# Optimization experiments

Measured on AMD Instinct MI355X. Metric: run time of the kernel, lower is better.

The kernel has to match this reference:

```python
import jax, jax.numpy as jnp
import numpy as np

B, L, C, D = 8, 8192, 256, 256


def setup_inputs() -> dict:
    key = jax.random.key(0)
    ks = jax.random.split(key, 13)
    bound = 1.0 / np.sqrt(C)

    def W(k):
        return jax.random.uniform(k, (C, D), jnp.float32, -bound, bound)

    def b(k):
        return jax.random.uniform(k, (D,), jnp.float32, -bound, bound)

    return {
        "xs": jax.random.normal(ks[0], (B, L, C), jnp.float32),
        # forward-direction params
        "Wh1": W(ks[1]), "bh1": b(ks[2]),
        "Wz1": W(ks[3]), "bz1": b(ks[4]),
        "Ws1": W(ks[5]), "bs1": b(ks[6]),
        "h01": jnp.zeros((1, 1, D), jnp.float32),
        # backward-direction params
        "Wh_1": W(ks[7]), "bh_1": b(ks[8]),
        "Wz_1": W(ks[9]), "bz_1": b(ks[10]),
        "Ws_1": W(ks[11]), "bs_1": b(ks[12]),
        "h0_1": jnp.zeros((1, 1, D), jnp.float32),
    }


def _gru_scan(z, h_tilde, h0):
    """h[t] = z[t]*h_tilde[t] + (1-z[t])*h[t-1], h[-1]=h0. Parallel over time
    via associative scan on the affine maps h -> a*h + b."""
    a = 1.0 - z            # [B, L, D]
    b = z * h_tilde        # [B, L, D]

    def combine(c1, c2):
        a1, b1 = c1
        a2, b2 = c2
        return a1 * a2, a2 * b1 + b2

    A, Bc = jax.lax.associative_scan(combine, (a, b), axis=1)
    return Bc + A * h0     # broadcast h0 [1,1,D]


def reference(xs, Wh1, bh1, Wz1, bz1, Ws1, bs1, h01,
              Wh_1, bh_1, Wz_1, bz_1, Ws_1, bs_1, h0_1):
    sig = jax.nn.sigmoid
    # forward direction
    hf = _gru_scan(sig(xs @ Wz1 + bz1), xs @ Wh1 + bh1, h01) * sig(xs @ Ws1 + bs1)
    # backward direction: reverse time, scan, reverse back
    zr = sig(xs @ Wz_1 + bz_1)
    hr = xs @ Wh_1 + bh_1
    hb = _gru_scan(zr[:, ::-1], hr[:, ::-1], h0_1)[:, ::-1] * sig(xs @ Ws_1 + bs_1)
    return hf + hb
```

## Files before the change

kernel.cpp:

```cpp
#include <hip/hip_runtime.h>
#include <hip/hip_bf16.h>

typedef unsigned short u16;

#define BDIM 8
#define LDIM 8192
#define KDIM 256
#define DDIM 256
#define MTOT 65536
#define NDIM 1536
#define TCH  32
#define NCH  256
#define NSUP 16


typedef float floatx4 __attribute__((ext_vector_type(4)));
typedef short bf16x8 __attribute__((ext_vector_type(8)));
typedef unsigned int u32x4 __attribute__((ext_vector_type(4)));
typedef unsigned int u32x2 __attribute__((ext_vector_type(2)));

__device__ __forceinline__ u16 f2bf(float f) {
  union { __hip_bfloat16 h; u16 u; } c;
  c.h = __float2bfloat16(f);
  return c.u;
}
__device__ __forceinline__ float bf2f(u16 u) {
  union { unsigned int i; float f; } c;
  c.i = ((unsigned int)u) << 16;
  return c.f;
}
__device__ __forceinline__ float sigmoidf_fast(float x) {
  return __builtin_amdgcn_rcpf(1.0f + __expf(-x));
}
__device__ __forceinline__ void gll16(const u16* g, u16* l) {
  __builtin_amdgcn_global_load_lds((const __attribute__((address_space(1))) void*)g,
                                   (__attribute__((address_space(3))) void*)l, 16, 0, 0);
}

__global__ void prep_conv(const float* __restrict__ Wh1, const float* __restrict__ Wz1,
                          const float* __restrict__ Ws1, const float* __restrict__ Wh_1,
                          const float* __restrict__ Wz_1, const float* __restrict__ Ws_1,
                          const float* __restrict__ bh1, const float* __restrict__ bz1,
                          const float* __restrict__ bs1, const float* __restrict__ bh_1,
                          const float* __restrict__ bz_1, const float* __restrict__ bs_1,
                          u16* __restrict__ WcatT, float* __restrict__ bcat,
                          const float* __restrict__ xs, u16* __restrict__ Abf) {
  if (blockIdx.x < NDIM) {
    const int n = blockIdx.x;
    const int k = threadIdx.x;
    const int nn = n & 63;
    const int p = (n & ~63) | ((nn & 15) << 2) | (nn >> 4);
    const int dir = p / 768, r = p % 768;
    int d; const float* W; const float* bb;
    if (r < 512) {
      d = r >> 1;
      if (r & 1) { W = dir ? Wz_1 : Wz1; bb = dir ? bz_1 : bz1; }
      else       { W = dir ? Wh_1 : Wh1; bb = dir ? bh_1 : bh1; }
    } else {
      d = r - 512;
      W = dir ? Ws_1 : Ws1; bb = dir ? bs_1 : bs1;
    }
    WcatT[(size_t)n * KDIM + k] = f2bf(W[k * DDIM + d]);
    if (k == 0) bcat[p] = bb[d];
  } else {
    const int cb = blockIdx.x - NDIM;
#pragma unroll
    for (int pass = 0; pass < 4; ++pass) {
      size_t i = ((size_t)(pass * 2048 + cb) * 256 + threadIdx.x) * 8;
      const float4* s = (const float4*)(xs + i);
      float4 f0 = s[0], f1 = s[1];
      union { u16 u[8]; u32x4 v; } t;
      t.u[0] = f2bf(f0.x); t.u[1] = f2bf(f0.y); t.u[2] = f2bf(f0.z); t.u[3] = f2bf(f0.w);
      t.u[4] = f2bf(f1.x); t.u[5] = f2bf(f1.y); t.u[6] = f2bf(f1.z); t.u[7] = f2bf(f1.w);
      *(u32x4*)(Abf + i) = t.v;
    }
  }
}

__global__ __launch_bounds__(256) void gemm_kernel(const u16* __restrict__ Abf,
                                                   const u16* __restrict__ WcatT,
                                                   const float* __restrict__ bcat,
                                                   u16* __restrict__ G,
                                                   float* __restrict__ Acc,
                                                   float* __restrict__ Bcc) {
  __shared__ __align__(16) u16 sm[16384];
  u16* As = sm;
  u16* Bs = sm + 8192;
  const int tid = threadIdx.x;
  const int lane = tid & 63, wave = tid >> 6;
  const int wm = wave >> 1, wn = wave & 1;
  const int q = lane >> 4, r = lane & 15;

  const int xcd = blockIdx.x & 7;
  const int li  = blockIdx.x >> 3;
  const int mt  = xcd * 64 + li / 12;
  const int nt  = li % 12;
  const int m0 = mt * 128, n0 = nt * 128;

  const u16* gA[4]; const u16* gB[4]; u16* lA[4]; u16* lB[4];
#pragma unroll
  for (int j = 0; j < 4; j++) {
    const int bi = wave * 256 + j * 64 + lane;
    const int row = bi >> 3;
    const int kq = (bi & 7) ^ (row & 7);
    gA[j] = Abf   + (size_t)(m0 + row) * KDIM + kq * 8;
    gB[j] = WcatT + (size_t)(n0 + row) * KDIM + kq * 8;
    lA[j] = As + bi * 8;
    lB[j] = Bs + bi * 8;
  }

  floatx4 acc[4][4];
  floatx4 z4 = {0.f, 0.f, 0.f, 0.f};
#pragma unroll
  for (int i = 0; i < 4; i++)
#pragma unroll
    for (int j = 0; j < 4; j++) acc[i][j] = z4;

  for (int k0 = 0; k0 < KDIM; k0 += 64) {
#pragma unroll
    for (int j = 0; j < 4; j++) { gll16(gA[j] + k0, lA[j]); gll16(gB[j] + k0, lB[j]); }
    __syncthreads();
#pragma unroll
    for (int kk = 0; kk < 2; kk++) {
      bf16x8 af[4], bv[4];
#pragma unroll
      for (int i = 0; i < 4; i++) {
        const int row = wm * 64 + i * 16 + r;
        af[i] = *(const bf16x8*)(As + (row * 8 + ((kk * 4 + q) ^ (row & 7))) * 8);
      }
#pragma unroll
      for (int j = 0; j < 4; j++) {
        const int row = wn * 64 + j * 16 + r;
        bv[j] = *(const bf16x8*)(Bs + (row * 8 + ((kk * 4 + q) ^ (row & 7))) * 8);
      }
#pragma unroll
      for (int i = 0; i < 4; i++)
#pragma unroll
        for (int j = 0; j < 4; j++)
          acc[i][j] = __builtin_amdgcn_mfma_f32_16x16x32_bf16(af[i], bv[j], acc[i][j], 0, 0, 0);
    }
    __syncthreads();
  }

  const int pcol = wn * 64 + (r << 2);
  const float4 bv4 = *(const float4*)(bcat + n0 + pcol);
  const int hz = (n0 % 768) < 512;

  if (hz) {
#pragma unroll
    for (int i = 0; i < 4; i++) {
#pragma unroll
      for (int reg = 0; reg < 4; reg++) {
        const int lrow = wm * 64 + i * 16 + q * 4 + reg;
        union { u16 u[4]; u32x2 v; } t;
        t.u[0] = f2bf(acc[i][0][reg] + bv4.x);
        t.u[1] = f2bf(acc[i][1][reg] + bv4.y);
        t.u[2] = f2bf(acc[i][2][reg] + bv4.z);
        t.u[3] = f2bf(acc[i][3][reg] + bv4.w);
        *(u32x2*)(sm + lrow * 128 + pcol) = t.v;
      }
    }

    __syncthreads();

#pragma unroll
    for (int p = 0; p < 8; p++) {
      const int idx = p * 2048 + tid * 8;
      const int row = idx >> 7, col = idx & 127;
      const u32x4 v = *(const u32x4*)(sm + idx);
      *(u32x4*)(G + (size_t)(m0 + row) * NDIM + n0 + col) = v;
    }

    const int cc = wave;
    const int dd = lane;
    const int dirn = n0 / 768;
    const int dbase = (n0 % 768) >> 1;
    const int bb = m0 >> 13;
    const int c0 = (m0 & 8191) >> 5;
    float h = 0.f, P = 1.f;
#pragma unroll 8
    for (int i = 0; i < TCH; ++i) {
      const int tl = dirn ? (TCH - 1 - i) : i;
      const unsigned int hzv = *(const unsigned int*)(sm + (cc * 32 + tl) * 128 + dd * 2);
      const float z = sigmoidf_fast(bf2f((u16)(hzv >> 16)));
      const float a = 1.f - z;
      h = fmaf(a, h, z * bf2f((u16)(hzv & 0xffffu)));
      P *= a;
    }
    const size_t u = (size_t)dirn * 2048 + (size_t)bb * 256 + (size_t)(c0 + cc);
    Acc[u * 256 + dbase + dd] = P;
    Bcc[u * 256 + dbase + dd] = h;
  } else {
#pragma unroll
    for (int i = 0; i < 4; i++) {
#pragma unroll
      for (int reg = 0; reg < 4; reg++) {
        const int lrow = wm * 64 + i * 16 + q * 4 + reg;
        union { u16 u[4]; u32x2 v; } t;
        t.u[0] = f2bf(acc[i][0][reg] + bv4.x);
        t.u[1] = f2bf(acc[i][1][reg] + bv4.y);
        t.u[2] = f2bf(acc[i][2][reg] + bv4.z);
        t.u[3] = f2bf(acc[i][3][reg] + bv4.w);
        *(u32x2*)(G + (size_t)(m0 + lrow) * NDIM + n0 + pcol) = t.v;
      }
    }
  }
}

__global__ __launch_bounds__(256) void scan_phaseB1(float* __restrict__ Acc,
                                                    float* __restrict__ Bcc,
                                                    float* __restrict__ Asum,
                                                    float* __restrict__ Bsum) {
  const int d = threadIdx.x;
  const int s   = blockIdx.x & 15;
  const int b   = (blockIdx.x >> 4) & 7;
  const int dir = blockIdx.x >> 7;
  const size_t ubase = ((size_t)dir * BDIM + b) * NCH;
  float a[16], bb[16];
#pragma unroll
  for (int i = 0; i < 16; ++i) {
    const int c = dir ? (NCH - 1 - (s * 16 + i)) : (s * 16 + i);
    const size_t idx = (ubase + c) * DDIM + d;
    a[i] = Acc[idx]; bb[i] = Bcc[idx];
  }
  float A = 1.f, Bv = 0.f;
#pragma unroll
  for (int i = 0; i < 16; ++i) {
    const int c = dir ? (NCH - 1 - (s * 16 + i)) : (s * 16 + i);
    const size_t idx = (ubase + c) * DDIM + d;
    Acc[idx] = A; Bcc[idx] = Bv;
    Bv = fmaf(a[i], Bv, bb[i]);
    A  = a[i] * A;
  }
  const size_t sidx = (((size_t)dir * BDIM + b) * NSUP + s) * DDIM + d;
  Asum[sidx] = A; Bsum[sidx] = Bv;
}

__global__ __launch_bounds__(256) void scan_phaseC(const u16* __restrict__ G,
                                                   const float* __restrict__ Acc,
                                                   const float* __restrict__ Bcc,
                                                   const float* __restrict__ Asum,
                                                   const float* __restrict__ Bsum,
                                                   const float* __restrict__ h01,
                                                   const float* __restrict__ h0_1,
                                                   float* __restrict__ out) {
  __shared__ float obuf[TCH * 256];
  const int c = blockIdx.x & 255, b = blockIdx.x >> 8;
  const int dir = threadIdx.x >> 7;
  const int ld  = threadIdx.x & 127;
  const int d0 = ld * 2;

  const int sp = dir ? ((NCH - 1 - c) >> 4) : (c >> 4);
  const float2 hh = dir ? *(const float2*)(h0_1 + d0) : *(const float2*)(h01 + d0);
  float ha = hh.x, hb = hh.y;
  const size_t sbase = ((size_t)dir * BDIM + b) * NSUP;
  for (int s = 0; s < sp; ++s) {
    const float2 As2 = *(const float2*)(Asum + (sbase + s) * DDIM + d0);
    const float2 Bs2 = *(const float2*)(Bsum + (sbase + s) * DDIM + d0);
    ha = fmaf(As2.x, ha, Bs2.x);
    hb = fmaf(As2.y, hb, Bs2.y);
  }
  const int u = dir * 2048 + b * 256 + c;
  const float2 ap = *(const float2*)(Acc + (size_t)u * 256 + d0);
  const float2 bp = *(const float2*)(Bcc + (size_t)u * 256 + d0);
  float h0 = fmaf(ap.x, ha, bp.x);
  float h1 = fmaf(ap.y, hb, bp.y);

  const u16* ghz = G + (size_t)b * LDIM * NDIM + dir * 768 + d0 * 2;
  const u16* gs  = G + (size_t)b * LDIM * NDIM + dir * 768 + 512 + d0;

  {
    uint2 hzr[16]; unsigned int sr[16];
#pragma unroll
    for (int i = 0; i < 16; ++i) {
      const int tl = dir ? (TCH - 1 - i) : i;
      const int t = c * TCH + tl;
      hzr[i] = *(const uint2*)(ghz + (size_t)t * NDIM);
      sr[i]  = *(const unsigned int*)(gs + (size_t)t * NDIM);
    }
#pragma unroll
    for (int i = 0; i < 16; ++i) {
      const int tl = dir ? (TCH - 1 - i) : i;
      const float z0 = sigmoidf_fast(bf2f((u16)(hzr[i].x >> 16)));
      const float z1 = sigmoidf_fast(bf2f((u16)(hzr[i].y >> 16)));
      h0 = fmaf(1.f - z0, h0, z0 * bf2f((u16)(hzr[i].x & 0xffffu)));
      h1 = fmaf(1.f - z1, h1, z1 * bf2f((u16)(hzr[i].y & 0xffffu)));
      float2 o;
      o.x = h0 * sigmoidf_fast(bf2f((u16)(sr[i] & 0xffffu)));
      o.y = h1 * sigmoidf_fast(bf2f((u16)(sr[i] >> 16)));
      *(float2*)(obuf + tl * 256 + d0) = o;
    }
  }

  __syncthreads();

  {
    uint2 hzr[16]; unsigned int sr[16];
#pragma unroll
    for (int i = 0; i < 16; ++i) {
      const int tl = dir ? (TCH - 1 - (16 + i)) : (16 + i);
      const int t = c * TCH + tl;
      hzr[i] = *(const uint2*)(ghz + (size_t)t * NDIM);
      sr[i]  = *(const unsigned int*)(gs + (size_t)t * NDIM);
    }
#pragma unroll
    for (int i = 0; i < 16; ++i) {
      const int tl = dir ? (TCH - 1 - (16 + i)) : (16 + i);
      const int t = c * TCH + tl;
      const float z0 = sigmoidf_fast(bf2f((u16)(hzr[i].x >> 16)));
      const float z1 = sigmoidf_fast(bf2f((u16)(hzr[i].y >> 16)));
      h0 = fmaf(1.f - z0, h0, z0 * bf2f((u16)(hzr[i].x & 0xffffu)));
      h1 = fmaf(1.f - z1, h1, z1 * bf2f((u16)(hzr[i].y & 0xffffu)));
      const float o0 = h0 * sigmoidf_fast(bf2f((u16)(sr[i] & 0xffffu)));
      const float o1 = h1 * sigmoidf_fast(bf2f((u16)(sr[i] >> 16)));
      const float2 other = *(const float2*)(obuf + tl * 256 + d0);
      float2 res;
      res.x = o0 + other.x;
      res.y = o1 + other.y;
      *(float2*)(out + ((size_t)b * LDIM + t) * DDIM + d0) = res;
    }
  }
}

extern "C" void kernel_launch(void* const* d_in, const int* in_sizes, int n_in,
                              void* d_out, int out_size, void* d_ws, size_t ws_size,
                              hipStream_t stream) {
  const float* xs   = (const float*)d_in[0];
  const float* Wh1  = (const float*)d_in[1];
  const float* bh1  = (const float*)d_in[2];
  const float* Wz1  = (const float*)d_in[3];
  const float* bz1  = (const float*)d_in[4];
  const float* Ws1  = (const float*)d_in[5];
  const float* bs1  = (const float*)d_in[6];
  const float* h01  = (const float*)d_in[7];
  const float* Wh_1 = (const float*)d_in[8];
  const float* bh_1 = (const float*)d_in[9];
  const float* Wz_1 = (const float*)d_in[10];
  const float* bz_1 = (const float*)d_in[11];
  const float* Ws_1 = (const float*)d_in[12];
  const float* bs_1 = (const float*)d_in[13];
  const float* h0_1 = (const float*)d_in[14];
  float* out = (float*)d_out;

  char* ws = (char*)d_ws;
  u16* WcatT = (u16*)ws;   ws += (size_t)NDIM * KDIM * 2;
  float* bcat = (float*)ws; ws += (size_t)NDIM * 4;
  u16* Abf = (u16*)ws;     ws += (size_t)MTOT * KDIM * 2;
  u16* G = (u16*)ws;       ws += (size_t)MTOT * NDIM * 2;

  const size_t sumElems = (size_t)2 * BDIM * NCH * DDIM;
  const size_t supElems = (size_t)2 * BDIM * NSUP * DDIM;
  float* Acc  = (float*)ws; ws += sumElems * 4;
  float* Bcc  = (float*)ws; ws += sumElems * 4;
  float* Asum = (float*)ws; ws += supElems * 4;
  float* Bsum = (float*)ws; ws += supElems * 4;
  if ((size_t)(ws - (char*)d_ws) > ws_size) return;

  prep_conv<<<dim3(NDIM + 2048), dim3(256), 0, stream>>>(
      Wh1, Wz1, Ws1, Wh_1, Wz_1, Ws_1, bh1, bz1, bs1, bh_1, bz_1, bs_1,
      WcatT, bcat, xs, Abf);
  gemm_kernel<<<dim3(6144), dim3(256), 0, stream>>>(Abf, WcatT, bcat, G, Acc, Bcc);
  scan_phaseB1<<<dim3(256), dim3(DDIM), 0, stream>>>(Acc, Bcc, Asum, Bsum);
  scan_phaseC<<<dim3(2048), dim3(256), 0, stream>>>(G, Acc, Bcc, Asum, Bsum, h01, h0_1, out);
}
```

Before: 270.8 us.

## Fuse fp32-to-bf16 input conversion into GEMM tile loads

Removes the separate pass that converted xs to a bf16 buffer and instead loads fp32 tiles of xs directly into LDS, converting to bf16 when building MFMA fragments. This drops a full read and write of the activations and one workspace buffer. In exchange, the GEMM moves twice the A-tile bytes through global and L2 memory and LDS per k-step, repeats the conversion for every n-tile, and uses more shared memory per block, which may reduce occupancy.

```diff
diff --git a/kernel.cpp b/kernel.cpp
--- a/kernel.cpp
+++ b/kernel.cpp
@@ -32,60 +32,45 @@
 __device__ __forceinline__ float sigmoidf_fast(float x) {
   return __builtin_amdgcn_rcpf(1.0f + __expf(-x));
 }
-__device__ __forceinline__ void gll16(const u16* g, u16* l) {
+__device__ __forceinline__ void gll16(const void* g, void* l) {
   __builtin_amdgcn_global_load_lds((const __attribute__((address_space(1))) void*)g,
                                    (__attribute__((address_space(3))) void*)l, 16, 0, 0);
 }
 
-__global__ void prep_conv(const float* __restrict__ Wh1, const float* __restrict__ Wz1,
-                          const float* __restrict__ Ws1, const float* __restrict__ Wh_1,
-                          const float* __restrict__ Wz_1, const float* __restrict__ Ws_1,
-                          const float* __restrict__ bh1, const float* __restrict__ bz1,
-                          const float* __restrict__ bs1, const float* __restrict__ bh_1,
-                          const float* __restrict__ bz_1, const float* __restrict__ bs_1,
-                          u16* __restrict__ WcatT, float* __restrict__ bcat,
-                          const float* __restrict__ xs, u16* __restrict__ Abf) {
-  if (blockIdx.x < NDIM) {
-    const int n = blockIdx.x;
-    const int k = threadIdx.x;
-    const int nn = n & 63;
-    const int p = (n & ~63) | ((nn & 15) << 2) | (nn >> 4);
-    const int dir = p / 768, r = p % 768;
-    int d; const float* W; const float* bb;
-    if (r < 512) {
-      d = r >> 1;
-      if (r & 1) { W = dir ? Wz_1 : Wz1; bb = dir ? bz_1 : bz1; }
-      else       { W = dir ? Wh_1 : Wh1; bb = dir ? bh_1 : bh1; }
-    } else {
-      d = r - 512;
-      W = dir ? Ws_1 : Ws1; bb = dir ? bs_1 : bs1;
-    }
-    WcatT[(size_t)n * KDIM + k] = f2bf(W[k * DDIM + d]);
-    if (k == 0) bcat[p] = bb[d];
+__global__ void prep_weights(const float* __restrict__ Wh1, const float* __restrict__ Wz1,
+                             const float* __restrict__ Ws1, const float* __restrict__ Wh_1,
+                             const float* __restrict__ Wz_1, const float* __restrict__ Ws_1,
+                             const float* __restrict__ bh1, const float* __restrict__ bz1,
+                             const float* __restrict__ bs1, const float* __restrict__ bh_1,
+                             const float* __restrict__ bz_1, const float* __restrict__ bs_1,
+                             u16* __restrict__ WcatT, float* __restrict__ bcat) {
+  const int n = blockIdx.x;
+  const int k = threadIdx.x;
+  const int nn = n & 63;
+  const int p = (n & ~63) | ((nn & 15) << 2) | (nn >> 4);
+  const int dir = p / 768, r = p % 768;
+  int d; const float* W; const float* bb;
+  if (r < 512) {
+    d = r >> 1;
+    if (r & 1) { W = dir ? Wz_1 : Wz1; bb = dir ? bz_1 : bz1; }
+    else       { W = dir ? Wh_1 : Wh1; bb = dir ? bh_1 : bh1; }
   } else {
-    const int cb = blockIdx.x - NDIM;
-#pragma unroll
-    for (int pass = 0; pass < 4; ++pass) {
-      size_t i = ((size_t)(pass * 2048 + cb) * 256 + threadIdx.x) * 8;
-      const float4* s = (const float4*)(xs + i);
-      float4 f0 = s[0], f1 = s[1];
-      union { u16 u[8]; u32x4 v; } t;
-      t.u[0] = f2bf(f0.x); t.u[1] = f2bf(f0.y); t.u[2] = f2bf(f0.z); t.u[3] = f2bf(f0.w);
-      t.u[4] = f2bf(f1.x); t.u[5] = f2bf(f1.y); t.u[6] = f2bf(f1.z); t.u[7] = f2bf(f1.w);
-      *(u32x4*)(Abf + i) = t.v;
-    }
-  }
-}
-
-__global__ __launch_bounds__(256) void gemm_kernel(const u16* __restrict__ Abf,
+    d = r - 512;
+    W = dir ? Ws_1 : Ws1; bb = dir ? bs_1 : bs1;
+  }
+  WcatT[(size_t)n * KDIM + k] = f2bf(W[k * DDIM + d]);
+  if (k == 0) bcat[p] = bb[d];
+}
+
+__global__ __launch_bounds__(256) void gemm_kernel(const float* __restrict__ xs,
                                                    const u16* __restrict__ WcatT,
                                                    const float* __restrict__ bcat,
                                                    u16* __restrict__ G,
                                                    float* __restrict__ Acc,
                                                    float* __restrict__ Bcc) {
-  __shared__ __align__(16) u16 sm[16384];
-  u16* As = sm;
-  u16* Bs = sm + 8192;
+  __shared__ __align__(16) u16 sm[24576];
+  float* Asf = (float*)sm;
+  u16* Bs = sm + 16384;
   const int tid = threadIdx.x;
   const int lane = tid & 63, wave = tid >> 6;
   const int wm = wave >> 1, wn = wave & 1;
@@ -97,15 +82,22 @@
   const int nt  = li % 12;
   const int m0 = mt * 128, n0 = nt * 128;
 
-  const u16* gA[4]; const u16* gB[4]; u16* lA[4]; u16* lB[4];
+  const float* gA[8]; float* lA[8];
+#pragma unroll
+  for (int j = 0; j < 8; j++) {
+    const int bi = wave * 512 + j * 64 + lane;
+    const int row = bi >> 4;
+    const int kq = (bi & 15) ^ (row & 15);
+    gA[j] = xs + (size_t)(m0 + row) * KDIM + kq * 4;
+    lA[j] = Asf + bi * 4;
+  }
+  const u16* gB[4]; u16* lB[4];
 #pragma unroll
   for (int j = 0; j < 4; j++) {
     const int bi = wave * 256 + j * 64 + lane;
     const int row = bi >> 3;
     const int kq = (bi & 7) ^ (row & 7);
-    gA[j] = Abf   + (size_t)(m0 + row) * KDIM + kq * 8;
     gB[j] = WcatT + (size_t)(n0 + row) * KDIM + kq * 8;
-    lA[j] = As + bi * 8;
     lB[j] = Bs + bi * 8;
   }
 
@@ -118,7 +110,9 @@
 
   for (int k0 = 0; k0 < KDIM; k0 += 64) {
 #pragma unroll
-    for (int j = 0; j < 4; j++) { gll16(gA[j] + k0, lA[j]); gll16(gB[j] + k0, lB[j]); }
+    for (int j = 0; j < 4; j++) gll16(gB[j] + k0, lB[j]);
+#pragma unroll
+    for (int j = 0; j < 8; j++) gll16(gA[j] + k0, lA[j]);
     __syncthreads();
 #pragma unroll
     for (int kk = 0; kk < 2; kk++) {
@@ -126,7 +120,17 @@
 #pragma unroll
       for (int i = 0; i < 4; i++) {
         const int row = wm * 64 + i * 16 + r;
-        af[i] = *(const bf16x8*)(As + (row * 8 + ((kk * 4 + q) ^ (row & 7))) * 8);
+        const int jq = kk * 8 + q * 2;
+        const int p0 = jq ^ (row & 15);
+        const int p1 = (jq + 1) ^ (row & 15);
+        const floatx4 fa0 = *(const floatx4*)(Asf + (row * 16 + p0) * 4);
+        const floatx4 fa1 = *(const floatx4*)(Asf + (row * 16 + p1) * 4);
+        union { u16 u[8]; bf16x8 v; } ua;
+        ua.u[0] = f2bf(fa0[0]); ua.u[1] = f2bf(fa0[1]);
+        ua.u[2] = f2bf(fa0[2]); ua.u[3] = f2bf(fa0[3]);
+        ua.u[4] = f2bf(fa1[0]); ua.u[5] = f2bf(fa1[1]);
+        ua.u[6] = f2bf(fa1[2]); ua.u[7] = f2bf(fa1[3]);
+        af[i] = ua.v;
       }
 #pragma unroll
       for (int j = 0; j < 4; j++) {
@@ -345,7 +349,6 @@
   char* ws = (char*)d_ws;
   u16* WcatT = (u16*)ws;   ws += (size_t)NDIM * KDIM * 2;
   float* bcat = (float*)ws; ws += (size_t)NDIM * 4;
-  u16* Abf = (u16*)ws;     ws += (size_t)MTOT * KDIM * 2;
   u16* G = (u16*)ws;       ws += (size_t)MTOT * NDIM * 2;
 
   const size_t sumElems = (size_t)2 * BDIM * NCH * DDIM;
@@ -356,10 +359,9 @@
   float* Bsum = (float*)ws; ws += supElems * 4;
   if ((size_t)(ws - (char*)d_ws) > ws_size) return;
 
-  prep_conv<<<dim3(NDIM + 2048), dim3(256), 0, stream>>>(
-      Wh1, Wz1, Ws1, Wh_1, Wz_1, Ws_1, bh1, bz1, bs1, bh_1, bz_1, bs_1,
-      WcatT, bcat, xs, Abf);
-  gemm_kernel<<<dim3(6144), dim3(256), 0, stream>>>(Abf, WcatT, bcat, G, Acc, Bcc);
+  prep_weights<<<dim3(NDIM), dim3(KDIM), 0, stream>>>(
+      Wh1, Wz1, Ws1, Wh_1, Wz_1, Ws_1, bh1, bz1, bs1, bh_1, bz_1, bs_1, WcatT, bcat);
+  gemm_kernel<<<dim3(6144), dim3(256), 0, stream>>>(xs, WcatT, bcat, G, Acc, Bcc);
   scan_phaseB1<<<dim3(256), dim3(DDIM), 0, stream>>>(Acc, Bcc, Asum, Bsum);
   scan_phaseC<<<dim3(2048), dim3(256), 0, stream>>>(G, Acc, Bcc, Asum, Bsum, h01, h0_1, out);
 }
```

After: 288.4 us. +6.5%, slower.
